# Performance work log

Measured on AMD Instinct MI355X. Metric: run time of the kernel, lower is better.

The kernel has to match this reference:

```python
import jax, jax.numpy as jnp
import numpy as np

H = 4          # global_attention_heads
NL = 32        # num_landmark_tokens
STRIDE = 16    # landmark_stride
D = 3072       # hidden_size
HD = D // H    # head_dim = 768
SCALE = 1.0 / np.sqrt(HD).astype(np.float32)


def _landmark_indices(seq_len: int) -> jnp.ndarray:
    # torch: arange(0, seq_len, stride); if >NL, index with linspace(0, n-1, NL).long() (truncation)
    idx = np.arange(0, seq_len, STRIDE, dtype=np.int64)
    if len(idx) > NL:
        sel = np.linspace(0, len(idx) - 1, NL).astype(np.int64)  # truncates like torch long cast
        idx = idx[sel]
    return jnp.asarray(idx)


def _attn(q_in, kv_in, Wq, bq, Wk, bk, Wv, bv, Wo, bo):
    # shared QKV/O projections, standard multi-head attention q_in -> kv_in
    B, Lq, _ = q_in.shape
    Lk = kv_in.shape[1]
    Q = (q_in @ Wq + bq).reshape(B, Lq, H, HD)
    K = (kv_in @ Wk + bk).reshape(B, Lk, H, HD)
    V = (kv_in @ Wv + bv).reshape(B, Lk, H, HD)
    scores = jnp.einsum('bqhd,bkhd->bhqk', Q, K) * SCALE
    w = jax.nn.softmax(scores, axis=-1)  # dropout is identity in eval
    ctx = jnp.einsum('bhqk,bkhd->bqhd', w, V).reshape(B, Lq, D)
    return ctx @ Wo + bo


def setup_inputs() -> dict:
    key = jax.random.key(0)
    ks = jax.random.split(key, 10)
    B, S = 2, 8192
    s = 1.0 / np.sqrt(D).astype(np.float32)
    return {
        'hidden_states': jax.random.normal(ks[0], (B, S, D), jnp.float32),
        'landmark_emb': jax.random.normal(ks[1], (NL, D), jnp.float32),
        'Wq': jax.random.normal(ks[2], (D, D), jnp.float32) * s,
        'bq': jnp.zeros((D,), jnp.float32),
        'Wk': jax.random.normal(ks[3], (D, D), jnp.float32) * s,
        'bk': jnp.zeros((D,), jnp.float32),
        'Wv': jax.random.normal(ks[4], (D, D), jnp.float32) * s,
        'bv': jnp.zeros((D,), jnp.float32),
        'Wo': jax.random.normal(ks[5], (D, D), jnp.float32) * s,
        'bo': jnp.zeros((D,), jnp.float32),
    }


def reference(hidden_states, landmark_emb, Wq, bq, Wk, bk, Wv, bv, Wo, bo):
    B, S, _ = hidden_states.shape
    li = _landmark_indices(S)  # [NL], static
    # gather landmarks + learned landmark embeddings
    landmark_tokens = hidden_states[:, li, :] + landmark_emb[None]  # [B, NL, D]
    # all tokens attend to 32 landmarks
    global_out = _attn(hidden_states, landmark_tokens, Wq, bq, Wk, bk, Wv, bv, Wo, bo)  # [B,S,D]
    # landmarks attend to all tokens
    landmark_out = _attn(landmark_tokens, hidden_states, Wq, bq, Wk, bk, Wv, bv, Wo, bo)  # [B,NL,D]
    # scatter landmark outputs back (index_copy-style, replaces python loop)
    updated = hidden_states.at[:, li, :].set(landmark_out)
    return updated + global_out
```

## Files before the change

### kernel.cpp

```cpp
#include <hip/hip_runtime.h>
#include <stdint.h>

#define S_LEN   8192
#define DMODEL  3072
#define HDIM    768
#define NLM     32
#define MTOK    16384
#define MV      16448
#define MP      16512
#define NQKV    9216
#define KDIM    3072
#define NKT     48
#define SCALE_F 0.036084391824351615f

#define OFF_A    ((size_t)0)
#define OFF_WT   ((size_t)101449728)
#define OFF_QKV  ((size_t)176947200)
#define OFF_CTX  ((size_t)480116736)
#define OFF_BCAT ((size_t)581566464)
#define OFF_PART ((size_t)581615616)
#define OFF_KT   (OFF_PART)
#define OFF_VT   (OFF_PART + 393216)
#define OFF_ML2  (OFF_PART + 786432)
#define OFF_CP   (OFF_A)

#if defined(__has_builtin)
#if __has_builtin(__builtin_amdgcn_global_load_lds)
#define USE_GLL 1
#endif
#endif
#ifndef USE_GLL
#define USE_GLL 0
#endif

typedef __attribute__((ext_vector_type(8))) short bf8_t;
typedef __attribute__((ext_vector_type(4))) float f4_t;
typedef __attribute__((ext_vector_type(4))) short s4_t;
typedef __attribute__((ext_vector_type(4))) unsigned short us4_t;

__device__ __forceinline__ float b2f(unsigned short u) {
  unsigned x = ((unsigned)u) << 16;
  float f;
  __builtin_memcpy(&f, &x, 4);
  return f;
}
__device__ __forceinline__ unsigned short f2b(float f) {
  unsigned x;
  __builtin_memcpy(&x, &f, 4);
  x += 0x7fffu + ((x >> 16) & 1u);
  return (unsigned short)(x >> 16);
}
__device__ __forceinline__ void load12(const unsigned short* p, float* f) {
  s4_t v0 = *(const s4_t*)p;
  s4_t v1 = *(const s4_t*)(p + 4);
  s4_t v2 = *(const s4_t*)(p + 8);
#pragma unroll
  for (int e = 0; e < 4; ++e) {
    f[e]     = b2f((unsigned short)v0[e]);
    f[4 + e] = b2f((unsigned short)v1[e]);
    f[8 + e] = b2f((unsigned short)v2[e]);
  }
}
__device__ __forceinline__ void store12(unsigned short* p, const float* f) {
  us4_t a = {f2b(f[0]), f2b(f[1]), f2b(f[2]), f2b(f[3])};
  us4_t b = {f2b(f[4]), f2b(f[5]), f2b(f[6]), f2b(f[7])};
  us4_t c = {f2b(f[8]), f2b(f[9]), f2b(f[10]), f2b(f[11])};
  *(us4_t*)p = a;
  *(us4_t*)(p + 4) = b;
  *(us4_t*)(p + 8) = c;
}

__global__ __launch_bounds__(256) void build_bcat(const float* __restrict__ bq,
                                                  const float* __restrict__ bk,
                                                  const float* __restrict__ bv,
                                                  const float* __restrict__ bo,
                                                  float* __restrict__ bcat) {
  int n = blockIdx.x * 256 + threadIdx.x;
  float v = (n < 3072) ? bq[n] : (n < 6144) ? bk[n - 3072]
          : (n < 9216) ? bv[n - 6144] : bo[n - 9216];
  bcat[n] = v;
}

__global__ __launch_bounds__(256) void build_a(const float* __restrict__ hs,
                                               const float* __restrict__ lemb,
                                               unsigned short* __restrict__ A) {
  size_t idx = (size_t)blockIdx.x * 256 + threadIdx.x;
  size_t e = idx * 4;
  int row = (int)(e / DMODEL);
  int col = (int)(e - (size_t)row * DMODEL);
  f4_t v;
  if (row < MTOK) {
    v = *(const f4_t*)(hs + e);
  } else if (row < MV) {
    int r2 = row - MTOK;
    int b = r2 >> 5, j = r2 & 31;
    int sel = (j * 511) / 31;
    int li = sel * 16;
    f4_t a = *(const f4_t*)(hs + ((size_t)(b * S_LEN + li)) * DMODEL + col);
    f4_t c = *(const f4_t*)(lemb + (size_t)j * DMODEL + col);
    v = a + c;
  } else {
    v = (f4_t){0.f, 0.f, 0.f, 0.f};
  }
  us4_t o = {f2b(v[0]), f2b(v[1]), f2b(v[2]), f2b(v[3])};
  *(us4_t*)(A + e) = o;
}

__global__ __launch_bounds__(256) void wtrans(const float* __restrict__ W,
                                              unsigned short* __restrict__ Wt) {
  __shared__ float t[32][33];
  int n0 = blockIdx.x * 32, k0 = blockIdx.y * 32;
  int x = threadIdx.x, y = threadIdx.y;
#pragma unroll
  for (int i = 0; i < 4; ++i)
    t[y + i * 8][x] = W[(size_t)(k0 + y + i * 8) * DMODEL + n0 + x];
  __syncthreads();
#pragma unroll
  for (int i = 0; i < 4; ++i)
    Wt[(size_t)(n0 + y + i * 8) * DMODEL + k0 + x] = f2b(t[x][y + i * 8]);
}

#if USE_GLL
#define GLL16(SRC, OFF)                                                        \
  __builtin_amdgcn_global_load_lds(                                           \
      (const __attribute__((address_space(1))) void*)(SRC),                   \
      (__attribute__((address_space(3))) void*)(lds + (OFF)), 16, 0, 0)
#else
#define GLL16(SRC, OFF)                                                        \
  (*(bf8_t*)(lds + (OFF) + (unsigned)(threadIdx.x & 63) * 16) = *(const bf8_t*)(SRC))
#endif

#define STG_A(TT, KH, DD)                                                      \
  do {                                                                         \
    const unsigned short* _s = gA0 + (size_t)(TT) * 64 + (KH) * 32;            \
    GLL16(_s, (unsigned)((DD) * 32768 + (KH) * 16384) + wl16);                 \
    GLL16(_s + (size_t)128 * KDIM,                                             \
          (unsigned)((DD) * 32768 + (KH) * 16384 + 8192) + wl16);              \
  } while (0)
#define STG_B(TT, KH, DD)                                                      \
  do {                                                                         \
    const unsigned short* _s = gB0 + (size_t)(TT) * 64 + (KH) * 32;            \
    GLL16(_s, (unsigned)(65536 + (DD) * 32768 + (KH) * 16384) + wl16);         \
    GLL16(_s + (size_t)128 * KDIM,                                             \
          (unsigned)(65536 + (DD) * 32768 + (KH) * 16384 + 8192) + wl16);      \
  } while (0)

#define LDA8(DD, KH, QM, MI)                                                   \
  (*(const bf8_t*)(lds + (DD) * 32768 + (KH) * 16384 + aBase + (QM) * 4096 +   \
                   (MI) * 1024))
#define LDB8(DD, KH, NI)                                                       \
  (*(const bf8_t*)(lds + (DD) * 32768 + (KH) * 16384 + bBase + (NI) * 1024))

#define MFMA16(Q)                                                              \
  do {                                                                         \
    __builtin_amdgcn_s_setprio(1);                                             \
    acc[(Q)+0][0] = __builtin_amdgcn_mfma_f32_16x16x32_bf16(a0, vb0, acc[(Q)+0][0], 0, 0, 0); \
    acc[(Q)+1][0] = __builtin_amdgcn_mfma_f32_16x16x32_bf16(a1, vb0, acc[(Q)+1][0], 0, 0, 0); \
    acc[(Q)+2][0] = __builtin_amdgcn_mfma_f32_16x16x32_bf16(a2, vb0, acc[(Q)+2][0], 0, 0, 0); \
    acc[(Q)+3][0] = __builtin_amdgcn_mfma_f32_16x16x32_bf16(a3, vb0, acc[(Q)+3][0], 0, 0, 0); \
    acc[(Q)+0][1] = __builtin_amdgcn_mfma_f32_16x16x32_bf16(a0, vb1, acc[(Q)+0][1], 0, 0, 0); \
    acc[(Q)+1][1] = __builtin_amdgcn_mfma_f32_16x16x32_bf16(a1, vb1, acc[(Q)+1][1], 0, 0, 0); \
    acc[(Q)+2][1] = __builtin_amdgcn_mfma_f32_16x16x32_bf16(a2, vb1, acc[(Q)+2][1], 0, 0, 0); \
    acc[(Q)+3][1] = __builtin_amdgcn_mfma_f32_16x16x32_bf16(a3, vb1, acc[(Q)+3][1], 0, 0, 0); \
    acc[(Q)+0][2] = __builtin_amdgcn_mfma_f32_16x16x32_bf16(a0, vb2, acc[(Q)+0][2], 0, 0, 0); \
    acc[(Q)+1][2] = __builtin_amdgcn_mfma_f32_16x16x32_bf16(a1, vb2, acc[(Q)+1][2], 0, 0, 0); \
    acc[(Q)+2][2] = __builtin_amdgcn_mfma_f32_16x16x32_bf16(a2, vb2, acc[(Q)+2][2], 0, 0, 0); \
    acc[(Q)+3][2] = __builtin_amdgcn_mfma_f32_16x16x32_bf16(a3, vb2, acc[(Q)+3][2], 0, 0, 0); \
    acc[(Q)+0][3] = __builtin_amdgcn_mfma_f32_16x16x32_bf16(a0, vb3, acc[(Q)+0][3], 0, 0, 0); \
    acc[(Q)+1][3] = __builtin_amdgcn_mfma_f32_16x16x32_bf16(a1, vb3, acc[(Q)+1][3], 0, 0, 0); \
    acc[(Q)+2][3] = __builtin_amdgcn_mfma_f32_16x16x32_bf16(a2, vb3, acc[(Q)+2][3], 0, 0, 0); \
    acc[(Q)+3][3] = __builtin_amdgcn_mfma_f32_16x16x32_bf16(a3, vb3, acc[(Q)+3][3], 0, 0, 0); \
    __builtin_amdgcn_s_setprio(0);                                             \
  } while (0)

__global__ __launch_bounds__(512, 2) void gemm256(const unsigned short* __restrict__ A,
                                                  const unsigned short* __restrict__ Bt,
                                                  const float* __restrict__ bias,
                                                  unsigned short* __restrict__ C,
                                                  int Mvalid, int N, int Ntiles) {
  extern __shared__ char lds[];
  const int tid = threadIdx.x;
  const int lane = tid & 63;
  const int wave = tid >> 6;
  const int WM = wave >> 2;
  const int WN = wave & 3;
  const int row16 = lane & 15, quad = lane >> 4;

  int nwg = (int)gridDim.x;
  int orig = (int)blockIdx.x;
  int q = nwg >> 3, r = nwg & 7;
  int xcd = orig & 7, lin = orig >> 3;
  int wg = (xcd < r ? xcd * (q + 1) : r * (q + 1) + (xcd - r) * q) + lin;
  const int tileM = (wg / Ntiles) * 256;
  const int tileN = (wg % Ntiles) * 256;

  const int srow2 = tid >> 2;
  const int scq = (tid & 3) ^ ((srow2 >> 1) & 3);
  const unsigned short* gA0 = A + (size_t)(tileM + srow2) * KDIM + scq * 8;
  const unsigned short* gB0 = Bt + (size_t)(tileN + srow2) * KDIM + scq * 8;
  const unsigned wl16 = (unsigned)(tid & 448) * 16;

  const unsigned co = (unsigned)((quad * 16) ^ (((row16 >> 1) & 3) << 4));
  const unsigned aBase = (unsigned)(WM * 8192 + row16 * 64) + co;
  const unsigned bBase = 65536u + (unsigned)(WN * 4096 + row16 * 64) + co;

  f4_t acc[8][4];
#pragma unroll
  for (int a = 0; a < 8; ++a)
#pragma unroll
    for (int b = 0; b < 4; ++b) acc[a][b] = (f4_t){0.f, 0.f, 0.f, 0.f};

  bf8_t vb0, vb1, vb2, vb3;

  STG_B(0, 0, 0); STG_A(0, 0, 0); STG_B(0, 1, 0); STG_A(0, 1, 0);
  STG_B(1, 0, 1); STG_A(1, 0, 1); STG_B(1, 1, 1);
  asm volatile("s_waitcnt vmcnt(6)" ::: "memory");
  __builtin_amdgcn_s_barrier();

#pragma unroll 2
  for (int t = 0; t < NKT; ++t) {
    const int d = t & 1;
    {
      bf8_t a0 = LDA8(d, 0, 0, 0), a1 = LDA8(d, 0, 0, 1),
            a2 = LDA8(d, 0, 0, 2), a3 = LDA8(d, 0, 0, 3);
      vb0 = LDB8(d, 0, 0); vb1 = LDB8(d, 0, 1);
      vb2 = LDB8(d, 0, 2); vb3 = LDB8(d, 0, 3);
      if (t + 1 < NKT) STG_A(t + 1, 1, d ^ 1);
      __builtin_amdgcn_s_barrier();
      asm volatile("s_waitcnt lgkmcnt(0)");
      MFMA16(0);
      __builtin_amdgcn_s_barrier();
    }
    {
      bf8_t a0 = LDA8(d, 0, 1, 0), a1 = LDA8(d, 0, 1, 1),
            a2 = LDA8(d, 0, 1, 2), a3 = LDA8(d, 0, 1, 3);
      if (t + 2 < NKT) STG_B(t + 2, 0, d);
      __builtin_amdgcn_s_barrier();
      asm volatile("s_waitcnt lgkmcnt(0)");
      MFMA16(4);
      __builtin_amdgcn_s_barrier();
    }
    {
      bf8_t a0 = LDA8(d, 1, 0, 0), a1 = LDA8(d, 1, 0, 1),
            a2 = LDA8(d, 1, 0, 2), a3 = LDA8(d, 1, 0, 3);
      vb0 = LDB8(d, 1, 0); vb1 = LDB8(d, 1, 1);
      vb2 = LDB8(d, 1, 2); vb3 = LDB8(d, 1, 3);
      if (t + 2 < NKT) STG_A(t + 2, 0, d);
      __builtin_amdgcn_s_barrier();
      asm volatile("s_waitcnt lgkmcnt(0)");
      MFMA16(0);
      __builtin_amdgcn_s_barrier();
    }
    {
      bf8_t a0 = LDA8(d, 1, 1, 0), a1 = LDA8(d, 1, 1, 1),
            a2 = LDA8(d, 1, 1, 2), a3 = LDA8(d, 1, 1, 3);
      if (t + 2 < NKT) STG_B(t + 2, 1, d);
      __builtin_amdgcn_s_barrier();
      asm volatile("s_waitcnt lgkmcnt(0)");
      MFMA16(4);
      if (t + 2 < NKT) asm volatile("s_waitcnt vmcnt(6)" ::: "memory");
      else             asm volatile("s_waitcnt vmcnt(0)" ::: "memory");
      __builtin_amdgcn_s_barrier();
    }
  }

  float bv_[4];
#pragma unroll
  for (int ni = 0; ni < 4; ++ni) bv_[ni] = bias[tileN + WN * 64 + ni * 16 + row16];
#pragma unroll
  for (int mi = 0; mi < 8; ++mi) {
#pragma unroll
    for (int i = 0; i < 4; ++i) {
      int grow = tileM + WM * 128 + mi * 16 + quad * 4 + i;
      if (grow < Mvalid) {
        size_t base = (size_t)grow * N + tileN + WN * 64 + row16;
#pragma unroll
        for (int ni = 0; ni < 4; ++ni)
          C[base + ni * 16] = f2b(acc[mi][ni][i] + bv_[ni]);
      }
    }
  }
}

__global__ __launch_bounds__(256) void kv_prep(const unsigned short* __restrict__ QKV,
                                               unsigned short* __restrict__ KT,
                                               unsigned short* __restrict__ VT) {
  int idx = blockIdx.x * 256 + threadIdx.x;
  if (idx < 24576) {
    int bh = idx / 3072, i = idx % 3072;
    int b = bh >> 2, h = bh & 3;
    int j = i & 31, c = i >> 5;
    bf8_t v = *(const bf8_t*)(QKV + (size_t)(MTOK + b * NLM + j) * NQKV + DMODEL +
                              h * HDIM + c * 8);
    *(bf8_t*)(KT + (size_t)bh * 24576 + (size_t)(c * 32 + j) * 8) = v;
  } else {
    int i2 = idx - 24576;
    int bh = i2 / 3072, r = i2 % 3072;
    int b = bh >> 2, h = bh & 3;
    int d = r >> 2, slot = r & 3;
    unsigned short vals[8];
#pragma unroll
    for (int e = 0; e < 8; ++e)
      vals[e] = QKV[(size_t)(MTOK + b * NLM + slot * 8 + e) * NQKV + 2 * DMODEL +
                    h * HDIM + d];
    unsigned short* p = VT + (size_t)bh * 24576 + (size_t)d * 32 + slot * 8;
    *(us4_t*)p = (us4_t){vals[0], vals[1], vals[2], vals[3]};
    *(us4_t*)(p + 4) = (us4_t){vals[4], vals[5], vals[6], vals[7]};
  }
}

__global__ __launch_bounds__(256, 2) void glob_attn(const unsigned short* __restrict__ QKV,
                                                    const unsigned short* __restrict__ KT,
                                                    const unsigned short* __restrict__ VT,
                                                    unsigned short* __restrict__ CTX) {
  __shared__ unsigned short P_s[4][32][32];
  const int tid = threadIdx.x;
  const int lane = tid & 63;
  const int w = tid >> 6;
  const int row16 = lane & 15, quad = lane >> 4;

  const int qt = blockIdx.x & 63;
  const int h = (blockIdx.x >> 6) & 3;
  const int b = blockIdx.x >> 8;
  const int bh = b * 4 + h;
  const int rowbase = b * S_LEN + qt * 128 + w * 32;

  const unsigned short* KTb = KT + (size_t)bh * 24576;
  const unsigned short* VTb = VT + (size_t)bh * 24576;

  f4_t sc[2][2];
#pragma unroll
  for (int mi = 0; mi < 2; ++mi)
#pragma unroll
    for (int ni = 0; ni < 2; ++ni) sc[mi][ni] = (f4_t){0.f, 0.f, 0.f, 0.f};

#pragma unroll
  for (int kt = 0; kt < 24; ++kt) {
    bf8_t kb0 = *(const bf8_t*)(KTb + (size_t)((kt * 4 + quad) * 32 + row16) * 8);
    bf8_t kb1 = *(const bf8_t*)(KTb + (size_t)((kt * 4 + quad) * 32 + 16 + row16) * 8);
    bf8_t qa0 = *(const bf8_t*)(QKV + (size_t)(rowbase + row16) * NQKV + h * HDIM +
                                kt * 32 + quad * 8);
    bf8_t qa1 = *(const bf8_t*)(QKV + (size_t)(rowbase + 16 + row16) * NQKV + h * HDIM +
                                kt * 32 + quad * 8);
    sc[0][0] = __builtin_amdgcn_mfma_f32_16x16x32_bf16(qa0, kb0, sc[0][0], 0, 0, 0);
    sc[0][1] = __builtin_amdgcn_mfma_f32_16x16x32_bf16(qa0, kb1, sc[0][1], 0, 0, 0);
    sc[1][0] = __builtin_amdgcn_mfma_f32_16x16x32_bf16(qa1, kb0, sc[1][0], 0, 0, 0);
    sc[1][1] = __builtin_amdgcn_mfma_f32_16x16x32_bf16(qa1, kb1, sc[1][1], 0, 0, 0);
  }

#pragma unroll
  for (int mi = 0; mi < 2; ++mi) {
#pragma unroll
    for (int i = 0; i < 4; ++i) {
      float s0 = sc[mi][0][i] * SCALE_F;
      float s1 = sc[mi][1][i] * SCALE_F;
      float mx = fmaxf(s0, s1);
#pragma unroll
      for (int off = 8; off; off >>= 1) mx = fmaxf(mx, __shfl_xor(mx, off));
      float p0 = __expf(s0 - mx), p1 = __expf(s1 - mx);
      float sum = p0 + p1;
#pragma unroll
      for (int off = 8; off; off >>= 1) sum += __shfl_xor(sum, off);
      float inv = 1.f / sum;
      int rr = mi * 16 + quad * 4 + i;
      P_s[w][rr][row16] = f2b(p0 * inv);
      P_s[w][rr][16 + row16] = f2b(p1 * inv);
    }
  }
  __syncthreads();

  bf8_t pa0 = *(const bf8_t*)&P_s[w][row16][quad * 8];
  bf8_t pa1 = *(const bf8_t*)&P_s[w][16 + row16][quad * 8];
  unsigned short* ctxb = CTX + (size_t)rowbase * DMODEL + h * HDIM;

#pragma unroll
  for (int dch = 0; dch < 12; ++dch) {
    bf8_t vb[4];
#pragma unroll
    for (int ni = 0; ni < 4; ++ni)
      vb[ni] = *(const bf8_t*)(VTb + (size_t)(dch * 64 + ni * 16 + row16) * 32 + quad * 8);
#pragma unroll
    for (int mi = 0; mi < 2; ++mi) {
      bf8_t pa = mi ? pa1 : pa0;
#pragma unroll
      for (int ni = 0; ni < 4; ++ni) {
        f4_t c = __builtin_amdgcn_mfma_f32_16x16x32_bf16(
            pa, vb[ni], (f4_t){0.f, 0.f, 0.f, 0.f}, 0, 0, 0);
#pragma unroll
        for (int i = 0; i < 4; ++i)
          ctxb[(size_t)(mi * 16 + quad * 4 + i) * DMODEL + dch * 64 + ni * 16 + row16] =
              f2b(c[i]);
      }
    }
  }
}

__global__ __launch_bounds__(256, 2) void lm_attn_part(const unsigned short* __restrict__ QKV,
                                                       float* __restrict__ ctxpart,
                                                       float* __restrict__ mlpart) {
  int wid = blockIdx.x * 4 + (threadIdx.x >> 6);
  int lane = threadIdx.x & 63;
  int kc = wid & 63, jg = (wid >> 6) & 3, h = (wid >> 8) & 3, b = wid >> 10;

  float qreg[8][12];
#pragma unroll
  for (int jj = 0; jj < 8; ++jj)
    load12(QKV + (size_t)(MTOK + b * NLM + jg * 8 + jj) * NQKV + h * HDIM + lane * 12,
           qreg[jj]);

  float m[8], l[8], ctx[8][12];
#pragma unroll
  for (int jj = 0; jj < 8; ++jj) {
    m[jj] = -1e30f;
    l[jj] = 0.f;
#pragma unroll
    for (int e = 0; e < 12; ++e) ctx[jj][e] = 0.f;
  }

  for (int k = kc * 128; k < kc * 128 + 128; ++k) {
    size_t row = (size_t)(b * S_LEN + k);
    float kv[12], vv[12];
    load12(QKV + row * NQKV + DMODEL + h * HDIM + lane * 12, kv);
    float s[8];
#pragma unroll
    for (int jj = 0; jj < 8; ++jj) {
      float p = 0.f;
#pragma unroll
      for (int e = 0; e < 12; ++e) p += qreg[jj][e] * kv[e];
      s[jj] = p;
    }
#pragma unroll
    for (int jj = 0; jj < 8; ++jj) {
#pragma unroll
      for (int off = 32; off; off >>= 1) s[jj] += __shfl_xor(s[jj], off);
      s[jj] *= SCALE_F;
    }
    load12(QKV + row * NQKV + 2 * DMODEL + h * HDIM + lane * 12, vv);
#pragma unroll
    for (int jj = 0; jj < 8; ++jj) {
      if (s[jj] <= m[jj]) {
        float pp = __expf(s[jj] - m[jj]);
        l[jj] += pp;
#pragma unroll
        for (int e = 0; e < 12; ++e) ctx[jj][e] += pp * vv[e];
      } else {
        float al = __expf(m[jj] - s[jj]);
        m[jj] = s[jj];
        l[jj] = l[jj] * al + 1.f;
#pragma unroll
        for (int e = 0; e < 12; ++e) ctx[jj][e] = ctx[jj][e] * al + vv[e];
      }
    }
  }

#pragma unroll
  for (int jj = 0; jj < 8; ++jj) {
    int p = (((b * 4 + h) * 32) + (jg * 8 + jj)) * 64 + kc;
    float* cp = ctxpart + (size_t)p * HDIM + lane * 12;
#pragma unroll
    for (int e = 0; e < 12; ++e) cp[e] = ctx[jj][e];
    if (lane == 0) {
      mlpart[p * 2] = m[jj];
      mlpart[p * 2 + 1] = l[jj];
    }
  }
}

__global__ __launch_bounds__(256) void lm_combine(const float* __restrict__ ctxpart,
                                                  const float* __restrict__ mlpart,
                                                  unsigned short* __restrict__ CTX) {
  int wid = blockIdx.x * 4 + (threadIdx.x >> 6);
  int lane = threadIdx.x & 63;
  int j = wid & 31, h = (wid >> 5) & 3, b = wid >> 7;
  int base = wid * 64;
  float mk = mlpart[(base + lane) * 2];
  float lk = mlpart[(base + lane) * 2 + 1];
  float mm = mk;
#pragma unroll
  for (int off = 32; off; off >>= 1) mm = fmaxf(mm, __shfl_xor(mm, off));
  float al = __expf(mk - mm);
  float ls = al * lk;
#pragma unroll
  for (int off = 32; off; off >>= 1) ls += __shfl_xor(ls, off);

  float ctx[12];
#pragma unroll
  for (int e = 0; e < 12; ++e) ctx[e] = 0.f;
  for (int kc = 0; kc < 64; ++kc) {
    float a = __shfl(al, kc);
    const float* cp = ctxpart + (size_t)(base + kc) * HDIM + lane * 12;
#pragma unroll
    for (int e = 0; e < 12; ++e) ctx[e] += a * cp[e];
  }
  float inv = 1.f / ls;
#pragma unroll
  for (int e = 0; e < 12; ++e) ctx[e] *= inv;
  store12(CTX + (size_t)(MTOK + b * NLM + j) * DMODEL + h * HDIM + lane * 12, ctx);
}

__global__ __launch_bounds__(256) void compose(const float* __restrict__ hs,
                                               const unsigned short* __restrict__ PROJ,
                                               float* __restrict__ out) {
  size_t idx = (size_t)blockIdx.x * 256 + threadIdx.x;
  size_t e = idx * 4;
  int row = (int)(e / DMODEL);
  int col = (int)(e - (size_t)row * DMODEL);
  int b = row >> 13, s = row & (S_LEN - 1);

  us4_t g4 = *(const us4_t*)(PROJ + (size_t)row * DMODEL + col);
  int j = -1;
  if ((s & 15) == 0) {
    int sel = s >> 4;
    int jc = (sel * 31 + 510) / 511;
    if (jc < 32 && (jc * 511) / 31 == sel) j = jc;
  }
  f4_t base;
  if (j >= 0) {
    us4_t l4 = *(const us4_t*)(PROJ + (size_t)(MTOK + b * NLM + j) * DMODEL + col);
    base = (f4_t){b2f(l4[0]), b2f(l4[1]), b2f(l4[2]), b2f(l4[3])};
  } else {
    base = *(const f4_t*)(hs + e);
  }
  f4_t o = {base[0] + b2f(g4[0]), base[1] + b2f(g4[1]),
            base[2] + b2f(g4[2]), base[3] + b2f(g4[3])};
  *(f4_t*)(out + e) = o;
}

extern "C" void kernel_launch(void* const* d_in, const int* in_sizes, int n_in,
                              void* d_out, int out_size, void* d_ws, size_t ws_size,
                              hipStream_t stream) {
  const float* hs   = (const float*)d_in[0];
  const float* lemb = (const float*)d_in[1];
  const float* Wq   = (const float*)d_in[2];
  const float* bq   = (const float*)d_in[3];
  const float* Wk   = (const float*)d_in[4];
  const float* bk   = (const float*)d_in[5];
  const float* Wv   = (const float*)d_in[6];
  const float* bv   = (const float*)d_in[7];
  const float* Wo   = (const float*)d_in[8];
  const float* bo   = (const float*)d_in[9];
  float* out = (float*)d_out;
  char* ws = (char*)d_ws;

  unsigned short* A    = (unsigned short*)(ws + OFF_A);
  unsigned short* Wt   = (unsigned short*)(ws + OFF_WT);
  unsigned short* QKV  = (unsigned short*)(ws + OFF_QKV);
  unsigned short* CTX  = (unsigned short*)(ws + OFF_CTX);
  float*          bcat = (float*)(ws + OFF_BCAT);
  unsigned short* KT   = (unsigned short*)(ws + OFF_KT);
  unsigned short* VT   = (unsigned short*)(ws + OFF_VT);
  float*          ml   = (float*)(ws + OFF_ML2);
  float*          cpart= (float*)(ws + OFF_CP);
  unsigned short* PROJ = (unsigned short*)(ws + OFF_A);

  static bool attr_set = false;
  if (!attr_set) {
    (void)hipFuncSetAttribute(reinterpret_cast<const void*>(gemm256),
                              hipFuncAttributeMaxDynamicSharedMemorySize, 131072);
    attr_set = true;
  }

  build_bcat<<<dim3(48), dim3(256), 0, stream>>>(bq, bk, bv, bo, bcat);
  build_a<<<dim3(49536), dim3(256), 0, stream>>>(hs, lemb, A);
  wtrans<<<dim3(96, 96), dim3(32, 8), 0, stream>>>(Wq, Wt);
  wtrans<<<dim3(96, 96), dim3(32, 8), 0, stream>>>(Wk, Wt + (size_t)3072 * KDIM);
  wtrans<<<dim3(96, 96), dim3(32, 8), 0, stream>>>(Wv, Wt + (size_t)6144 * KDIM);
  wtrans<<<dim3(96, 96), dim3(32, 8), 0, stream>>>(Wo, Wt + (size_t)9216 * KDIM);

  gemm256<<<dim3(65 * 36), dim3(512), 131072, stream>>>(A, Wt, bcat, QKV, MV, NQKV, 36);

  kv_prep<<<dim3(192), dim3(256), 0, stream>>>(QKV, KT, VT);
  glob_attn<<<dim3(512), dim3(256), 0, stream>>>(QKV, KT, VT, CTX);
  lm_attn_part<<<dim3(512), dim3(256), 0, stream>>>(QKV, cpart, ml);
  lm_combine<<<dim3(64), dim3(256), 0, stream>>>(cpart, ml, CTX);

  gemm256<<<dim3(65 * 12), dim3(512), 131072, stream>>>(
      CTX, Wt + (size_t)9216 * KDIM, bcat + 9216, PROJ, MV, DMODEL, 12);

  compose<<<dim3(49152), dim3(256), 0, stream>>>(hs, PROJ, out);
}
```

Baseline: 2.019 ms.

## Hoist LDS fragment loads, add grouped tile swizzle, reorder landmark warp mapping

The GEMM main loop now loads all A/B LDS fragments for a K-tile up front and drops the explicit lgkmcnt(0) waits, so the compiler can overlap LDS reads with MFMA work. Workgroups are also remapped into groups of 16 M-tiles that sweep N, which should improve L2 reuse of the weight tiles. In the landmark attention kernel, the query group index now varies fastest across waves, so neighbouring waves read the same K/V chunk. The cost is higher register pressure from holding about 24 fragments live, which could cause spills at 2 blocks per CU.

Result: slower. 3.193 ms (+58.1%).

```diff
diff --git a/kernel.cpp b/kernel.cpp
--- a/kernel.cpp
+++ b/kernel.cpp
@@ -151,25 +151,25 @@
 #define LDB8(DD, KH, NI)                                                       \
   (*(const bf8_t*)(lds + (DD) * 32768 + (KH) * 16384 + bBase + (NI) * 1024))
 
-#define MFMA16(Q)                                                              \
+#define MFMA16(Q, A0, A1, A2, A3, B0, B1, B2, B3)                              \
   do {                                                                         \
     __builtin_amdgcn_s_setprio(1);                                             \
-    acc[(Q)+0][0] = __builtin_amdgcn_mfma_f32_16x16x32_bf16(a0, vb0, acc[(Q)+0][0], 0, 0, 0); \
-    acc[(Q)+1][0] = __builtin_amdgcn_mfma_f32_16x16x32_bf16(a1, vb0, acc[(Q)+1][0], 0, 0, 0); \
-    acc[(Q)+2][0] = __builtin_amdgcn_mfma_f32_16x16x32_bf16(a2, vb0, acc[(Q)+2][0], 0, 0, 0); \
-    acc[(Q)+3][0] = __builtin_amdgcn_mfma_f32_16x16x32_bf16(a3, vb0, acc[(Q)+3][0], 0, 0, 0); \
-    acc[(Q)+0][1] = __builtin_amdgcn_mfma_f32_16x16x32_bf16(a0, vb1, acc[(Q)+0][1], 0, 0, 0); \
-    acc[(Q)+1][1] = __builtin_amdgcn_mfma_f32_16x16x32_bf16(a1, vb1, acc[(Q)+1][1], 0, 0, 0); \
-    acc[(Q)+2][1] = __builtin_amdgcn_mfma_f32_16x16x32_bf16(a2, vb1, acc[(Q)+2][1], 0, 0, 0); \
-    acc[(Q)+3][1] = __builtin_amdgcn_mfma_f32_16x16x32_bf16(a3, vb1, acc[(Q)+3][1], 0, 0, 0); \
-    acc[(Q)+0][2] = __builtin_amdgcn_mfma_f32_16x16x32_bf16(a0, vb2, acc[(Q)+0][2], 0, 0, 0); \
-    acc[(Q)+1][2] = __builtin_amdgcn_mfma_f32_16x16x32_bf16(a1, vb2, acc[(Q)+1][2], 0, 0, 0); \
-    acc[(Q)+2][2] = __builtin_amdgcn_mfma_f32_16x16x32_bf16(a2, vb2, acc[(Q)+2][2], 0, 0, 0); \
-    acc[(Q)+3][2] = __builtin_amdgcn_mfma_f32_16x16x32_bf16(a3, vb2, acc[(Q)+3][2], 0, 0, 0); \
-    acc[(Q)+0][3] = __builtin_amdgcn_mfma_f32_16x16x32_bf16(a0, vb3, acc[(Q)+0][3], 0, 0, 0); \
-    acc[(Q)+1][3] = __builtin_amdgcn_mfma_f32_16x16x32_bf16(a1, vb3, acc[(Q)+1][3], 0, 0, 0); \
-    acc[(Q)+2][3] = __builtin_amdgcn_mfma_f32_16x16x32_bf16(a2, vb3, acc[(Q)+2][3], 0, 0, 0); \
-    acc[(Q)+3][3] = __builtin_amdgcn_mfma_f32_16x16x32_bf16(a3, vb3, acc[(Q)+3][3], 0, 0, 0); \
+    acc[(Q)+0][0] = __builtin_amdgcn_mfma_f32_16x16x32_bf16(A0, B0, acc[(Q)+0][0], 0, 0, 0); \
+    acc[(Q)+1][0] = __builtin_amdgcn_mfma_f32_16x16x32_bf16(A1, B0, acc[(Q)+1][0], 0, 0, 0); \
+    acc[(Q)+2][0] = __builtin_amdgcn_mfma_f32_16x16x32_bf16(A2, B0, acc[(Q)+2][0], 0, 0, 0); \
+    acc[(Q)+3][0] = __builtin_amdgcn_mfma_f32_16x16x32_bf16(A3, B0, acc[(Q)+3][0], 0, 0, 0); \
+    acc[(Q)+0][1] = __builtin_amdgcn_mfma_f32_16x16x32_bf16(A0, B1, acc[(Q)+0][1], 0, 0, 0); \
+    acc[(Q)+1][1] = __builtin_amdgcn_mfma_f32_16x16x32_bf16(A1, B1, acc[(Q)+1][1], 0, 0, 0); \
+    acc[(Q)+2][1] = __builtin_amdgcn_mfma_f32_16x16x32_bf16(A2, B1, acc[(Q)+2][1], 0, 0, 0); \
+    acc[(Q)+3][1] = __builtin_amdgcn_mfma_f32_16x16x32_bf16(A3, B1, acc[(Q)+3][1], 0, 0, 0); \
+    acc[(Q)+0][2] = __builtin_amdgcn_mfma_f32_16x16x32_bf16(A0, B2, acc[(Q)+0][2], 0, 0, 0); \
+    acc[(Q)+1][2] = __builtin_amdgcn_mfma_f32_16x16x32_bf16(A1, B2, acc[(Q)+1][2], 0, 0, 0); \
+    acc[(Q)+2][2] = __builtin_amdgcn_mfma_f32_16x16x32_bf16(A2, B2, acc[(Q)+2][2], 0, 0, 0); \
+    acc[(Q)+3][2] = __builtin_amdgcn_mfma_f32_16x16x32_bf16(A3, B2, acc[(Q)+3][2], 0, 0, 0); \
+    acc[(Q)+0][3] = __builtin_amdgcn_mfma_f32_16x16x32_bf16(A0, B3, acc[(Q)+0][3], 0, 0, 0); \
+    acc[(Q)+1][3] = __builtin_amdgcn_mfma_f32_16x16x32_bf16(A1, B3, acc[(Q)+1][3], 0, 0, 0); \
+    acc[(Q)+2][3] = __builtin_amdgcn_mfma_f32_16x16x32_bf16(A2, B3, acc[(Q)+2][3], 0, 0, 0); \
+    acc[(Q)+3][3] = __builtin_amdgcn_mfma_f32_16x16x32_bf16(A3, B3, acc[(Q)+3][3], 0, 0, 0); \
     __builtin_amdgcn_s_setprio(0);                                             \
   } while (0)
 
@@ -177,7 +177,8 @@
                                                   const unsigned short* __restrict__ Bt,
                                                   const float* __restrict__ bias,
                                                   unsigned short* __restrict__ C,
-                                                  int Mvalid, int N, int Ntiles) {
+                                                  int Mvalid, int N,
+                                                  int Mtiles, int Ntiles) {
   extern __shared__ char lds[];
   const int tid = threadIdx.x;
   const int lane = tid & 63;
@@ -191,8 +192,17 @@
   int q = nwg >> 3, r = nwg & 7;
   int xcd = orig & 7, lin = orig >> 3;
   int wg = (xcd < r ? xcd * (q + 1) : r * (q + 1) + (xcd - r) * q) + lin;
-  const int tileM = (wg / Ntiles) * 256;
-  const int tileN = (wg % Ntiles) * 256;
+
+  const int SMg = 16;
+  int spg = SMg * Ntiles;
+  int g = wg / spg;
+  int within = wg - g * spg;
+  int sm = Mtiles - g * SMg;
+  if (sm > SMg) sm = SMg;
+  int n_ = within / sm;
+  int m_ = within - n_ * sm;
+  const int tileM = (g * SMg + m_) * 256;
+  const int tileN = n_ * 256;
 
   const int srow2 = tid >> 2;
   const int scq = (tid & 3) ^ ((srow2 >> 1) & 3);
@@ -210,8 +220,6 @@
 #pragma unroll
     for (int b = 0; b < 4; ++b) acc[a][b] = (f4_t){0.f, 0.f, 0.f, 0.f};
 
-  bf8_t vb0, vb1, vb2, vb3;
-
   STG_B(0, 0, 0); STG_A(0, 0, 0); STG_B(0, 1, 0); STG_A(0, 1, 0);
   STG_B(1, 0, 1); STG_A(1, 0, 1); STG_B(1, 1, 1);
   asm volatile("s_waitcnt vmcnt(6)" ::: "memory");
@@ -220,44 +228,40 @@
 #pragma unroll 2
   for (int t = 0; t < NKT; ++t) {
     const int d = t & 1;
+    bf8_t a00 = LDA8(d, 0, 0, 0), a01 = LDA8(d, 0, 0, 1),
+          a02 = LDA8(d, 0, 0, 2), a03 = LDA8(d, 0, 0, 3);
+    bf8_t b00 = LDB8(d, 0, 0), b01 = LDB8(d, 0, 1),
+          b02 = LDB8(d, 0, 2), b03 = LDB8(d, 0, 3);
+    bf8_t a10 = LDA8(d, 0, 1, 0), a11 = LDA8(d, 0, 1, 1),
+          a12 = LDA8(d, 0, 1, 2), a13 = LDA8(d, 0, 1, 3);
+    bf8_t a20 = LDA8(d, 1, 0, 0), a21 = LDA8(d, 1, 0, 1),
+          a22 = LDA8(d, 1, 0, 2), a23 = LDA8(d, 1, 0, 3);
+    bf8_t b10 = LDB8(d, 1, 0), b11 = LDB8(d, 1, 1),
+          b12 = LDB8(d, 1, 2), b13 = LDB8(d, 1, 3);
+    bf8_t a30 = LDA8(d, 1, 1, 0), a31 = LDA8(d, 1, 1, 1),
+          a32 = LDA8(d, 1, 1, 2), a33 = LDA8(d, 1, 1, 3);
     {
-      bf8_t a0 = LDA8(d, 0, 0, 0), a1 = LDA8(d, 0, 0, 1),
-            a2 = LDA8(d, 0, 0, 2), a3 = LDA8(d, 0, 0, 3);
-      vb0 = LDB8(d, 0, 0); vb1 = LDB8(d, 0, 1);
-      vb2 = LDB8(d, 0, 2); vb3 = LDB8(d, 0, 3);
       if (t + 1 < NKT) STG_A(t + 1, 1, d ^ 1);
       __builtin_amdgcn_s_barrier();
-      asm volatile("s_waitcnt lgkmcnt(0)");
-      MFMA16(0);
+      MFMA16(0, a00, a01, a02, a03, b00, b01, b02, b03);
       __builtin_amdgcn_s_barrier();
     }
     {
-      bf8_t a0 = LDA8(d, 0, 1, 0), a1 = LDA8(d, 0, 1, 1),
-            a2 = LDA8(d, 0, 1, 2), a3 = LDA8(d, 0, 1, 3);
       if (t + 2 < NKT) STG_B(t + 2, 0, d);
       __builtin_amdgcn_s_barrier();
-      asm volatile("s_waitcnt lgkmcnt(0)");
-      MFMA16(4);
+      MFMA16(4, a10, a11, a12, a13, b00, b01, b02, b03);
       __builtin_amdgcn_s_barrier();
     }
     {
-      bf8_t a0 = LDA8(d, 1, 0, 0), a1 = LDA8(d, 1, 0, 1),
-            a2 = LDA8(d, 1, 0, 2), a3 = LDA8(d, 1, 0, 3);
-      vb0 = LDB8(d, 1, 0); vb1 = LDB8(d, 1, 1);
-      vb2 = LDB8(d, 1, 2); vb3 = LDB8(d, 1, 3);
       if (t + 2 < NKT) STG_A(t + 2, 0, d);
       __builtin_amdgcn_s_barrier();
-      asm volatile("s_waitcnt lgkmcnt(0)");
-      MFMA16(0);
+      MFMA16(0, a20, a21, a22, a23, b10, b11, b12, b13);
       __builtin_amdgcn_s_barrier();
     }
     {
-      bf8_t a0 = LDA8(d, 1, 1, 0), a1 = LDA8(d, 1, 1, 1),
-            a2 = LDA8(d, 1, 1, 2), a3 = LDA8(d, 1, 1, 3);
       if (t + 2 < NKT) STG_B(t + 2, 1, d);
       __builtin_amdgcn_s_barrier();
-      asm volatile("s_waitcnt lgkmcnt(0)");
-      MFMA16(4);
+      MFMA16(4, a30, a31, a32, a33, b10, b11, b12, b13);
       if (t + 2 < NKT) asm volatile("s_waitcnt vmcnt(6)" ::: "memory");
       else             asm volatile("s_waitcnt vmcnt(0)" ::: "memory");
       __builtin_amdgcn_s_barrier();
@@ -400,7 +404,7 @@
                                                        float* __restrict__ mlpart) {
   int wid = blockIdx.x * 4 + (threadIdx.x >> 6);
   int lane = threadIdx.x & 63;
-  int kc = wid & 63, jg = (wid >> 6) & 3, h = (wid >> 8) & 3, b = wid >> 10;
+  int jg = wid & 3, kc = (wid >> 2) & 63, h = (wid >> 8) & 3, b = wid >> 10;
 
   float qreg[8][12];
 #pragma unroll
@@ -567,7 +571,7 @@
   wtrans<<<dim3(96, 96), dim3(32, 8), 0, stream>>>(Wv, Wt + (size_t)6144 * KDIM);
   wtrans<<<dim3(96, 96), dim3(32, 8), 0, stream>>>(Wo, Wt + (size_t)9216 * KDIM);
 
-  gemm256<<<dim3(65 * 36), dim3(512), 131072, stream>>>(A, Wt, bcat, QKV, MV, NQKV, 36);
+  gemm256<<<dim3(65 * 36), dim3(512), 131072, stream>>>(A, Wt, bcat, QKV, MV, NQKV, 65, 36);
 
   kv_prep<<<dim3(192), dim3(256), 0, stream>>>(QKV, KT, VT);
   glob_attn<<<dim3(512), dim3(256), 0, stream>>>(QKV, KT, VT, CTX);
@@ -575,7 +579,7 @@
   lm_combine<<<dim3(64), dim3(256), 0, stream>>>(cpart, ml, CTX);
 
   gemm256<<<dim3(65 * 12), dim3(512), 131072, stream>>>(
-      CTX, Wt + (size_t)9216 * KDIM, bcat + 9216, PROJ, MV, DMODEL, 12);
+      CTX, Wt + (size_t)9216 * KDIM, bcat + 9216, PROJ, MV, DMODEL, 65, 12);
 
   compose<<<dim3(49152), dim3(256), 0, stream>>>(hs, PROJ, out);
 }
```
